# Performance work log

Measured on AMD Instinct MI355X. Metric: run time of the kernel, lower is better.

## Reference

```python
import jax, jax.numpy as jnp
import numpy as np
import math

SIZE = 64
NLAND = 8
N_ITER = 6


def setup_inputs() -> dict:
    key = jax.random.key(0)
    k1, k2, k3 = jax.random.split(key, 3)
    B, T, C = 4, 4096, 1024
    return {
        "q": jax.random.normal(k1, (B, T, C), dtype=jnp.float32),
        "k": jax.random.normal(k2, (B, T, C), dtype=jnp.float32),
        "v": jax.random.normal(k3, (B, T, C), dtype=jnp.float32),
    }


def _iterative_pinv(mat, n_iter=N_ITER):
    # Newton-Schulz iteration for pseudo-inverse of [..., m, m] kernel.
    m = mat.shape[-1]
    I = jnp.eye(m, dtype=mat.dtype)
    K = mat
    # NOTE: torch.max over the whole tensor (global scalar), faithful to source.
    V = (1.0 / jnp.max(jnp.sum(K, axis=-2))) * jnp.swapaxes(K, -1, -2)
    for _ in range(n_iter):
        KV = jnp.matmul(K, V)
        V = jnp.matmul(0.25 * V, 13.0 * I - jnp.matmul(KV, 15.0 * I - jnp.matmul(KV, 7.0 * I - KV)))
    return V


def reference(q, k, v):
    B, T, C = q.shape
    H = C // SIZE
    scale = 1.0 / math.sqrt(SIZE)
    # Faithful reshape (not transpose) as in the source module.
    qh = q.reshape(B, H, T, SIZE)
    kh = k.reshape(B, H, T, SIZE)
    vh = v.reshape(B, H, T, SIZE)
    # T % NLAND == 0 branch: landmark = segment mean over T//NLAND tokens.
    q_l = qh.reshape(B, H, NLAND, T // NLAND, SIZE).mean(axis=-2)  # [B,H,m,d]
    k_l = kh.reshape(B, H, NLAND, T // NLAND, SIZE).mean(axis=-2)
    kernel_1 = jax.nn.softmax(jnp.einsum('bhtd,bhmd->bhtm', qh, k_l) * scale, axis=-1)  # [B,H,T,m]
    kernel_2 = jax.nn.softmax(jnp.einsum('bhmd,bhnd->bhmn', q_l, k_l) * scale, axis=-1)  # [B,H,m,m]
    kernel_3 = jax.nn.softmax(jnp.einsum('bhmd,bhtd->bhmt', q_l, kh) * scale, axis=-1)  # [B,H,m,T]
    pinv = _iterative_pinv(kernel_2)  # [B,H,m,m]
    k3v = jnp.matmul(kernel_3, vh)    # [B,H,m,d]
    out = jnp.matmul(jnp.matmul(kernel_1, pinv), k3v)  # [B,H,T,d]
    return out.reshape(B, T, C)
```

## Files before the change

### kernel.cpp

```cpp
#include <hip/hip_runtime.h>
#include <math.h>

#define T_TOK 4096
#define DD 64
#define NHEADS 64
#define SEG 512
#define NCHUNK 32
#define CHUNK 128
#define SCALE 0.125f

#define QL_OFF   0
#define KL_OFF   32768
#define K2_OFF   65536
#define CS_OFF   69632
#define KP_OFF   70144
#define PA_OFF   70144
#define PD_OFF   1118720
#define W2_OFF   1135104
#define P_OFF    1167872

#define WAVE_BAR() __builtin_amdgcn_wave_barrier()

__global__ __launch_bounds__(256) void qsum_kernel(
    const float* __restrict__ q, float* __restrict__ ws) {
  int tid = threadIdx.x;
  const float4* q4 = (const float4*)q + (size_t)blockIdx.x * 8192;
  float4 b[2][8];
#pragma unroll
  for (int i = 0; i < 8; ++i) b[0][i] = q4[i * 256 + tid];
  float4 a = make_float4(0.f, 0.f, 0.f, 0.f);
#pragma unroll
  for (int j = 0; j < 4; ++j) {
    if (j < 3) {
#pragma unroll
      for (int i = 0; i < 8; ++i)
        b[(j + 1) & 1][i] = q4[(j + 1) * 2048 + i * 256 + tid];
    }
#pragma unroll
    for (int i = 0; i < 8; ++i) {
      float4 x = b[j & 1][i];
      a.x += x.x; a.y += x.y; a.z += x.z; a.w += x.w;
    }
  }
  __shared__ float4 red[16][17];
  red[tid >> 4][tid & 15] = a;
  __syncthreads();
  if (tid < 16) {
    float4 s = make_float4(0.f, 0.f, 0.f, 0.f);
#pragma unroll
    for (int g = 0; g < 16; ++g) {
      float4 r = red[g][tid];
      s.x += r.x; s.y += r.y; s.z += r.z; s.w += r.w;
    }
    const float inv = 1.f / (float)SEG;
    s.x *= inv; s.y *= inv; s.z *= inv; s.w *= inv;
    ((float4*)(ws + QL_OFF))[blockIdx.x * 16 + tid] = s;
  }
}

__global__ __launch_bounds__(256) void ppass_kernel(
    const float* __restrict__ k, float* __restrict__ ws) {
  int tid = threadIdx.x;
  int w = tid >> 6, lane = tid & 63;
  int gw = blockIdx.x * 4 + w;
  int hb = gw >> 6;
  __shared__ float kt_all[4][16][68];
  float (*kt)[68] = kt_all[w];

  int m = lane & 7;
  float4 qlrow[16];
#pragma unroll
  for (int d4 = 0; d4 < 16; ++d4)
    qlrow[d4] = ((const float4*)(ws + QL_OFF))[hb * 128 + m * 16 + d4];

  size_t tokbase = (size_t)gw * 64;
  const float4* k4 = (const float4*)k + tokbase * 16;
  float4 buf[2][4];
#pragma unroll
  for (int i = 0; i < 4; ++i) buf[0][i] = k4[i * 64 + lane];
  float4 ks = make_float4(0.f, 0.f, 0.f, 0.f);

#pragma unroll
  for (int tile = 0; tile < 4; ++tile) {
    int cur = tile & 1;
    if (tile < 3) {
#pragma unroll
      for (int i = 0; i < 4; ++i)
        buf[cur ^ 1][i] = k4[(tile + 1) * 256 + i * 64 + lane];
    }
#pragma unroll
    for (int i = 0; i < 4; ++i) {
      int f4 = i * 64 + lane;
      *(float4*)&kt[f4 >> 4][(f4 & 15) * 4] = buf[cur][i];
      ks.x += buf[cur][i].x; ks.y += buf[cur][i].y;
      ks.z += buf[cur][i].z; ks.w += buf[cur][i].w;
    }
    WAVE_BAR();
#pragma unroll
    for (int rep = 0; rep < 2; ++rep) {
      int t = rep * 8 + (lane >> 3);
      const float4* kr = (const float4*)&kt[t][0];
      float dp = 0.f;
#pragma unroll
      for (int d4 = 0; d4 < 16; ++d4) {
        float4 kv = kr[d4];
        dp += kv.x * qlrow[d4].x + kv.y * qlrow[d4].y +
              kv.z * qlrow[d4].z + kv.w * qlrow[d4].w;
      }
      ws[P_OFF + (tokbase + tile * 16 + t) * 8 + m] = __expf(dp * SCALE);
    }
    WAVE_BAR();
  }
  ks.x += __shfl_xor(ks.x, 16, 64); ks.y += __shfl_xor(ks.y, 16, 64);
  ks.z += __shfl_xor(ks.z, 16, 64); ks.w += __shfl_xor(ks.w, 16, 64);
  ks.x += __shfl_xor(ks.x, 32, 64); ks.y += __shfl_xor(ks.y, 32, 64);
  ks.z += __shfl_xor(ks.z, 32, 64); ks.w += __shfl_xor(ks.w, 32, 64);
  if (lane < 16)
    ((float4*)(ws + KP_OFF))[gw * 16 + lane] = ks;
}

__global__ __launch_bounds__(512) void prepk_kernel(float* __restrict__ ws) {
  int hb = blockIdx.x, tid = threadIdx.x;
  __shared__ float qls[8][68];
  __shared__ float kls[8][68];
  __shared__ float ee[8][9];
  int m = tid >> 6, d = tid & 63;
  float s = 0.f;
#pragma unroll
  for (int j = 0; j < 8; ++j)
    s += ws[KP_OFF + (size_t)(hb * 64 + m * 8 + j) * 64 + d];
  s *= (1.f / (float)SEG);
  kls[m][d] = s;
  ws[KL_OFF + hb * 512 + tid] = s;
  qls[m][d] = ws[QL_OFF + hb * 512 + tid];
  __syncthreads();
  if (tid < 64) {
    int i = tid >> 3, j = tid & 7;
    float dot = 0.f;
#pragma unroll
    for (int dd = 0; dd < 64; ++dd) dot += qls[i][dd] * kls[j][dd];
    ee[i][j] = __expf(dot * SCALE);
  }
  __syncthreads();
  if (tid < 64) {
    int i = tid >> 3, j = tid & 7;
    float ssum = 0.f;
#pragma unroll
    for (int jj = 0; jj < 8; ++jj) ssum += ee[i][jj];
    ws[K2_OFF + hb * 64 + tid] = ee[i][j] / ssum;
  }
  if (tid < 8) {
    float cs = 0.f;
    for (int ii = 0; ii < 8; ++ii) {
      float ssum = 0.f;
#pragma unroll
      for (int jj = 0; jj < 8; ++jj) ssum += ee[ii][jj];
      cs += ee[ii][tid] / ssum;
    }
    ws[CS_OFF + hb * 8 + tid] = cs;
  }
}

__global__ __launch_bounds__(256) void vpass_kernel(
    const float* __restrict__ v, float* __restrict__ ws) {
  int tid = threadIdx.x;
  int w = tid >> 6, lane = tid & 63, g = lane >> 4;
  int hb = blockIdx.x >> 5, c = blockIdx.x & 31;

  size_t tokbase = (size_t)hb * T_TOK + (size_t)c * CHUNK + (size_t)w * 32;
  float4 pf = ((const float4*)(ws + P_OFF))[tokbase * 2 + lane];
  const float4* v4 = (const float4*)v + tokbase * 16;
  float4 vv[8];
#pragma unroll
  for (int it = 0; it < 8; ++it) vv[it] = v4[it * 64 + lane];

  __shared__ float plds[4][260];
  *(float4*)&plds[w][lane * 4] = pf;
  WAVE_BAR();

  float4 acc[8];
#pragma unroll
  for (int m = 0; m < 8; ++m) acc[m] = make_float4(0.f, 0.f, 0.f, 0.f);

#pragma unroll
  for (int it = 0; it < 8; ++it) {
    int t = it * 4 + g;
    float4 pa = *(const float4*)&plds[w][t * 8];
    float4 pb = *(const float4*)&plds[w][t * 8 + 4];
    acc[0].x += pa.x * vv[it].x; acc[0].y += pa.x * vv[it].y; acc[0].z += pa.x * vv[it].z; acc[0].w += pa.x * vv[it].w;
    acc[1].x += pa.y * vv[it].x; acc[1].y += pa.y * vv[it].y; acc[1].z += pa.y * vv[it].z; acc[1].w += pa.y * vv[it].w;
    acc[2].x += pa.z * vv[it].x; acc[2].y += pa.z * vv[it].y; acc[2].z += pa.z * vv[it].z; acc[2].w += pa.z * vv[it].w;
    acc[3].x += pa.w * vv[it].x; acc[3].y += pa.w * vv[it].y; acc[3].z += pa.w * vv[it].z; acc[3].w += pa.w * vv[it].w;
    acc[4].x += pb.x * vv[it].x; acc[4].y += pb.x * vv[it].y; acc[4].z += pb.x * vv[it].z; acc[4].w += pb.x * vv[it].w;
    acc[5].x += pb.y * vv[it].x; acc[5].y += pb.y * vv[it].y; acc[5].z += pb.y * vv[it].z; acc[5].w += pb.y * vv[it].w;
    acc[6].x += pb.z * vv[it].x; acc[6].y += pb.z * vv[it].y; acc[6].z += pb.z * vv[it].z; acc[6].w += pb.z * vv[it].w;
    acc[7].x += pb.w * vv[it].x; acc[7].y += pb.w * vv[it].y; acc[7].z += pb.w * vv[it].z; acc[7].w += pb.w * vv[it].w;
  }
#pragma unroll
  for (int m = 0; m < 8; ++m) {
#pragma unroll
    for (int s = 16; s <= 32; s <<= 1) {
      acc[m].x += __shfl_xor(acc[m].x, s, 64);
      acc[m].y += __shfl_xor(acc[m].y, s, 64);
      acc[m].z += __shfl_xor(acc[m].z, s, 64);
      acc[m].w += __shfl_xor(acc[m].w, s, 64);
    }
  }
  __shared__ float4 accs[4][8][17];
  __shared__ float dens[4][8];
  if (lane < 16) {
#pragma unroll
    for (int m = 0; m < 8; ++m) accs[w][m][lane] = acc[m];
  }
  if (lane < 8) {
    float dsum = 0.f;
#pragma unroll
    for (int t = 0; t < 32; ++t) dsum += plds[w][t * 8 + lane];
    dens[w][lane] = dsum;
  }
  __syncthreads();
  if (tid < 128) {
    int m = tid >> 4, i = tid & 15;
    float4 a = accs[0][m][i], b = accs[1][m][i], cc = accs[2][m][i], dd = accs[3][m][i];
    float4 s = make_float4(a.x + b.x + cc.x + dd.x, a.y + b.y + cc.y + dd.y,
                           a.z + b.z + cc.z + dd.z, a.w + b.w + cc.w + dd.w);
    ((float4*)(ws + PA_OFF))[((size_t)(hb * 32 + c) * 8 + m) * 16 + i] = s;
  }
  if (tid < 8)
    ws[PD_OFF + (hb * NCHUNK + c) * 8 + tid] =
        dens[0][tid] + dens[1][tid] + dens[2][tid] + dens[3][tid];
}

__global__ __launch_bounds__(512) void pinvw2_kernel(float* __restrict__ ws) {
  int hb = blockIdx.x, tid = threadIdx.x;
  __shared__ float k3vs[8][68];
  __shared__ float K[8][9], V[8][9], X[8][9], Y[8][9];
  __shared__ float smax;
  int m = tid >> 6, d = tid & 63;
  float s = 0.f, den = 0.f;
  for (int c = 0; c < NCHUNK; ++c) {
    s += ws[PA_OFF + (((size_t)hb * NCHUNK + c) * 8 + m) * 64 + d];
    den += ws[PD_OFF + (hb * NCHUNK + c) * 8 + m];
  }
  k3vs[m][d] = s / den;
  if (tid < 64) {
    float mx = 0.f;
    for (int t = 0; t < 8; ++t) mx = fmaxf(mx, ws[CS_OFF + t * 64 + tid]);
    for (int off = 32; off; off >>= 1) mx = fmaxf(mx, __shfl_xor(mx, off, 64));
    if (tid == 0) smax = mx;
  }
  int i = (tid >> 3) & 7, j = tid & 7;
  if (tid < 64) K[i][j] = ws[K2_OFF + hb * 64 + tid];
  __syncthreads();
  if (tid < 64) V[i][j] = K[j][i] * (1.f / smax);
  __syncthreads();
  for (int it = 0; it < 6; ++it) {
    float x = 0.f;
    if (tid < 64) {
      for (int kk = 0; kk < 8; ++kk) x += K[i][kk] * V[kk][j];
      X[i][j] = x;
    }
    __syncthreads();
    float bm = 0.f;
    if (tid < 64) {
      for (int kk = 0; kk < 8; ++kk) bm += X[i][kk] * X[kk][j];
      bm = 7.f * x - bm;
      Y[i][j] = bm;
    }
    __syncthreads();
    float dm = 0.f;
    if (tid < 64) {
      for (int kk = 0; kk < 8; ++kk) dm += X[i][kk] * Y[kk][j];
      dm = 15.f * x - dm;
    }
    __syncthreads();
    if (tid < 64) Y[i][j] = dm;
    __syncthreads();
    float vd = 0.f;
    if (tid < 64) {
      for (int kk = 0; kk < 8; ++kk) vd += V[i][kk] * Y[kk][j];
      vd = 0.25f * (13.f * V[i][j] - vd);
    }
    __syncthreads();
    if (tid < 64) V[i][j] = vd;
    __syncthreads();
  }
  float o = 0.f;
#pragma unroll
  for (int jj = 0; jj < 8; ++jj) o += V[m][jj] * k3vs[jj][d];
  ws[W2_OFF + hb * 512 + tid] = o;
}

__global__ __launch_bounds__(256) void out_kernel(
    const float* __restrict__ q, float* __restrict__ out,
    const float* __restrict__ ws) {
  int tid = threadIdx.x;
  int w = tid >> 6, lane = tid & 63;
  int gw = blockIdx.x * 4 + w;
  int hb = gw >> 6;
  __shared__ float qt_all[4][16][68];
  __shared__ float pl_all[4][16][9];
  __shared__ float w2_all[4][8][68];
  float (*qt)[68] = qt_all[w];
  float (*pl)[9]  = pl_all[w];
  float (*w2)[68] = w2_all[w];

  int m = lane & 7;
  float4 klrow[16];
#pragma unroll
  for (int d4 = 0; d4 < 16; ++d4)
    klrow[d4] = ((const float4*)(ws + KL_OFF))[hb * 128 + m * 16 + d4];
#pragma unroll
  for (int i = 0; i < 2; ++i) {
    int f4 = i * 64 + lane;
    float4 y = ((const float4*)(ws + W2_OFF))[hb * 128 + f4];
    *(float4*)&w2[f4 >> 4][(f4 & 15) * 4] = y;
  }

  size_t base4 = (size_t)gw * 1024;
  const float4* q4 = (const float4*)q + base4;
  float4* o4 = (float4*)out + base4;
  float4 buf[2][4];
#pragma unroll
  for (int i = 0; i < 4; ++i) buf[0][i] = q4[i * 64 + lane];

#pragma unroll
  for (int tile = 0; tile < 4; ++tile) {
    int cur = tile & 1;
    if (tile < 3) {
#pragma unroll
      for (int i = 0; i < 4; ++i)
        buf[cur ^ 1][i] = q4[(tile + 1) * 256 + i * 64 + lane];
    }
#pragma unroll
    for (int i = 0; i < 4; ++i) {
      int f4 = i * 64 + lane;
      *(float4*)&qt[f4 >> 4][(f4 & 15) * 4] = buf[cur][i];
    }
    WAVE_BAR();
#pragma unroll
    for (int rep = 0; rep < 2; ++rep) {
      int t = rep * 8 + (lane >> 3);
      const float4* qr = (const float4*)&qt[t][0];
      float dot = 0.f;
#pragma unroll
      for (int d4 = 0; d4 < 16; ++d4) {
        float4 a = qr[d4];
        dot += a.x * klrow[d4].x + a.y * klrow[d4].y +
               a.z * klrow[d4].z + a.w * klrow[d4].w;
      }
      pl[t][m] = __expf(dot * SCALE);
    }
    WAVE_BAR();
#pragma unroll
    for (int i = 0; i < 4; ++i) {
      int t = i * 4 + (lane >> 4);
      int qd = lane & 15;
      float p0 = pl[t][0], p1 = pl[t][1], p2 = pl[t][2], p3 = pl[t][3];
      float p4 = pl[t][4], p5 = pl[t][5], p6 = pl[t][6], p7 = pl[t][7];
      float inv = 1.f / (p0 + p1 + p2 + p3 + p4 + p5 + p6 + p7);
      float4 acc = make_float4(0.f, 0.f, 0.f, 0.f);
      float pm[8] = {p0, p1, p2, p3, p4, p5, p6, p7};
#pragma unroll
      for (int m2 = 0; m2 < 8; ++m2) {
        float wgt = pm[m2] * inv;
        float4 wv = *(const float4*)&w2[m2][qd * 4];
        acc.x += wgt * wv.x; acc.y += wgt * wv.y;
        acc.z += wgt * wv.z; acc.w += wgt * wv.w;
      }
      o4[tile * 256 + i * 64 + lane] = acc;
    }
    WAVE_BAR();
  }
}

extern "C" void kernel_launch(void* const* d_in, const int* in_sizes, int n_in,
                              void* d_out, int out_size, void* d_ws, size_t ws_size,
                              hipStream_t stream) {
  const float* q = (const float*)d_in[0];
  const float* k = (const float*)d_in[1];
  const float* v = (const float*)d_in[2];
  float* out = (float*)d_out;
  float* ws = (float*)d_ws;

  qsum_kernel<<<512, 256, 0, stream>>>(q, ws);
  ppass_kernel<<<1024, 256, 0, stream>>>(k, ws);
  prepk_kernel<<<NHEADS, 512, 0, stream>>>(ws);
  vpass_kernel<<<NHEADS * NCHUNK, 256, 0, stream>>>(v, ws);
  pinvw2_kernel<<<NHEADS, 512, 0, stream>>>(ws);
  out_kernel<<<1024, 256, 0, stream>>>(q, out, ws);
}
```

Before: 88.76 us.

## Fuse K-score pass and V accumulation into a single kv-pass kernel

Merges the ppass and vpass kernels so each wave computes the exp scores for its 64 tokens and immediately accumulates the exp-weighted V sums and denominators, instead of writing the P matrix to workspace and reading it back in a separate launch. The landmark query rows now live in shared memory rather than registers, which frees registers for the new V buffers and accumulators. The intent is to remove one launch and the global round trip for P. The cost is more per-wave partials (64 per head instead of 32) for pinvw2 to reduce, and higher register pressure in the fused kernel.

```diff
diff --git a/kernel.cpp b/kernel.cpp
--- a/kernel.cpp
+++ b/kernel.cpp
@@ -5,8 +5,6 @@
 #define DD 64
 #define NHEADS 64
 #define SEG 512
-#define NCHUNK 32
-#define CHUNK 128
 #define SCALE 0.125f
 
 #define QL_OFF   0
@@ -14,10 +12,9 @@
 #define K2_OFF   65536
 #define CS_OFF   69632
 #define KP_OFF   70144
-#define PA_OFF   70144
-#define PD_OFF   1118720
-#define W2_OFF   1135104
-#define P_OFF    1167872
+#define PA_OFF   332288
+#define PD_OFF   2429440
+#define W2_OFF   2462208
 
 #define WAVE_BAR() __builtin_amdgcn_wave_barrier()
 
@@ -58,56 +55,87 @@
   }
 }
 
-__global__ __launch_bounds__(256) void ppass_kernel(
-    const float* __restrict__ k, float* __restrict__ ws) {
+__global__ __launch_bounds__(256) void kvpass_kernel(
+    const float* __restrict__ k, const float* __restrict__ v,
+    float* __restrict__ ws) {
   int tid = threadIdx.x;
   int w = tid >> 6, lane = tid & 63;
   int gw = blockIdx.x * 4 + w;
   int hb = gw >> 6;
+  __shared__ float qls[8][68];
   __shared__ float kt_all[4][16][68];
+  __shared__ float pl_all[4][16][9];
   float (*kt)[68] = kt_all[w];
-
-  int m = lane & 7;
-  float4 qlrow[16];
-#pragma unroll
-  for (int d4 = 0; d4 < 16; ++d4)
-    qlrow[d4] = ((const float4*)(ws + QL_OFF))[hb * 128 + m * 16 + d4];
-
+  float (*pl)[9]  = pl_all[w];
+
+  if (tid < 128) {
+    float4 x = ((const float4*)(ws + QL_OFF))[hb * 128 + tid];
+    *(float4*)&qls[tid >> 4][(tid & 15) * 4] = x;
+  }
+  __syncthreads();
+
+  int m = lane & 7, g = lane >> 4;
   size_t tokbase = (size_t)gw * 64;
   const float4* k4 = (const float4*)k + tokbase * 16;
-  float4 buf[2][4];
-#pragma unroll
-  for (int i = 0; i < 4; ++i) buf[0][i] = k4[i * 64 + lane];
+  const float4* v4 = (const float4*)v + tokbase * 16;
+  float4 kb[2][4], vb[2][4];
+#pragma unroll
+  for (int i = 0; i < 4; ++i) { kb[0][i] = k4[i * 64 + lane]; vb[0][i] = v4[i * 64 + lane]; }
+
   float4 ks = make_float4(0.f, 0.f, 0.f, 0.f);
+  float den = 0.f;
+  float4 acc[8];
+#pragma unroll
+  for (int mm = 0; mm < 8; ++mm) acc[mm] = make_float4(0.f, 0.f, 0.f, 0.f);
 
 #pragma unroll
   for (int tile = 0; tile < 4; ++tile) {
     int cur = tile & 1;
     if (tile < 3) {
 #pragma unroll
-      for (int i = 0; i < 4; ++i)
-        buf[cur ^ 1][i] = k4[(tile + 1) * 256 + i * 64 + lane];
+      for (int i = 0; i < 4; ++i) {
+        kb[cur ^ 1][i] = k4[(tile + 1) * 256 + i * 64 + lane];
+        vb[cur ^ 1][i] = v4[(tile + 1) * 256 + i * 64 + lane];
+      }
     }
 #pragma unroll
     for (int i = 0; i < 4; ++i) {
       int f4 = i * 64 + lane;
-      *(float4*)&kt[f4 >> 4][(f4 & 15) * 4] = buf[cur][i];
-      ks.x += buf[cur][i].x; ks.y += buf[cur][i].y;
-      ks.z += buf[cur][i].z; ks.w += buf[cur][i].w;
+      *(float4*)&kt[f4 >> 4][(f4 & 15) * 4] = kb[cur][i];
+      ks.x += kb[cur][i].x; ks.y += kb[cur][i].y;
+      ks.z += kb[cur][i].z; ks.w += kb[cur][i].w;
     }
     WAVE_BAR();
 #pragma unroll
     for (int rep = 0; rep < 2; ++rep) {
       int t = rep * 8 + (lane >> 3);
       const float4* kr = (const float4*)&kt[t][0];
+      const float4* qr = (const float4*)&qls[m][0];
       float dp = 0.f;
 #pragma unroll
       for (int d4 = 0; d4 < 16; ++d4) {
-        float4 kv = kr[d4];
-        dp += kv.x * qlrow[d4].x + kv.y * qlrow[d4].y +
-              kv.z * qlrow[d4].z + kv.w * qlrow[d4].w;
+        float4 kv = kr[d4], qv = qr[d4];
+        dp += kv.x * qv.x + kv.y * qv.y + kv.z * qv.z + kv.w * qv.w;
       }
-      ws[P_OFF + (tokbase + tile * 16 + t) * 8 + m] = __expf(dp * SCALE);
+      float p = __expf(dp * SCALE);
+      pl[t][m] = p;
+      den += p;
+    }
+    WAVE_BAR();
+#pragma unroll
+    for (int i = 0; i < 4; ++i) {
+      int t = i * 4 + g;
+      float4 vv = vb[cur][i];
+      float p0 = pl[t][0], p1 = pl[t][1], p2 = pl[t][2], p3 = pl[t][3];
+      float p4 = pl[t][4], p5 = pl[t][5], p6 = pl[t][6], p7 = pl[t][7];
+      acc[0].x += p0 * vv.x; acc[0].y += p0 * vv.y; acc[0].z += p0 * vv.z; acc[0].w += p0 * vv.w;
+      acc[1].x += p1 * vv.x; acc[1].y += p1 * vv.y; acc[1].z += p1 * vv.z; acc[1].w += p1 * vv.w;
+      acc[2].x += p2 * vv.x; acc[2].y += p2 * vv.y; acc[2].z += p2 * vv.z; acc[2].w += p2 * vv.w;
+      acc[3].x += p3 * vv.x; acc[3].y += p3 * vv.y; acc[3].z += p3 * vv.z; acc[3].w += p3 * vv.w;
+      acc[4].x += p4 * vv.x; acc[4].y += p4 * vv.y; acc[4].z += p4 * vv.z; acc[4].w += p4 * vv.w;
+      acc[5].x += p5 * vv.x; acc[5].y += p5 * vv.y; acc[5].z += p5 * vv.z; acc[5].w += p5 * vv.w;
+      acc[6].x += p6 * vv.x; acc[6].y += p6 * vv.y; acc[6].z += p6 * vv.z; acc[6].w += p6 * vv.w;
+      acc[7].x += p7 * vv.x; acc[7].y += p7 * vv.y; acc[7].z += p7 * vv.z; acc[7].w += p7 * vv.w;
     }
     WAVE_BAR();
   }
@@ -117,6 +145,26 @@
   ks.z += __shfl_xor(ks.z, 32, 64); ks.w += __shfl_xor(ks.w, 32, 64);
   if (lane < 16)
     ((float4*)(ws + KP_OFF))[gw * 16 + lane] = ks;
+  den += __shfl_xor(den, 8, 64);
+  den += __shfl_xor(den, 16, 64);
+  den += __shfl_xor(den, 32, 64);
+  if (lane < 8)
+    ws[PD_OFF + (size_t)gw * 8 + lane] = den;
+#pragma unroll
+  for (int mm = 0; mm < 8; ++mm) {
+#pragma unroll
+    for (int s = 16; s <= 32; s <<= 1) {
+      acc[mm].x += __shfl_xor(acc[mm].x, s, 64);
+      acc[mm].y += __shfl_xor(acc[mm].y, s, 64);
+      acc[mm].z += __shfl_xor(acc[mm].z, s, 64);
+      acc[mm].w += __shfl_xor(acc[mm].w, s, 64);
+    }
+  }
+  if (lane < 16) {
+#pragma unroll
+    for (int mm = 0; mm < 8; ++mm)
+      ((float4*)(ws + PA_OFF))[((size_t)gw * 8 + mm) * 16 + lane] = acc[mm];
+  }
 }
 
 __global__ __launch_bounds__(512) void prepk_kernel(float* __restrict__ ws) {
@@ -161,76 +209,6 @@
   }
 }
 
-__global__ __launch_bounds__(256) void vpass_kernel(
-    const float* __restrict__ v, float* __restrict__ ws) {
-  int tid = threadIdx.x;
-  int w = tid >> 6, lane = tid & 63, g = lane >> 4;
-  int hb = blockIdx.x >> 5, c = blockIdx.x & 31;
-
-  size_t tokbase = (size_t)hb * T_TOK + (size_t)c * CHUNK + (size_t)w * 32;
-  float4 pf = ((const float4*)(ws + P_OFF))[tokbase * 2 + lane];
-  const float4* v4 = (const float4*)v + tokbase * 16;
-  float4 vv[8];
-#pragma unroll
-  for (int it = 0; it < 8; ++it) vv[it] = v4[it * 64 + lane];
-
-  __shared__ float plds[4][260];
-  *(float4*)&plds[w][lane * 4] = pf;
-  WAVE_BAR();
-
-  float4 acc[8];
-#pragma unroll
-  for (int m = 0; m < 8; ++m) acc[m] = make_float4(0.f, 0.f, 0.f, 0.f);
-
-#pragma unroll
-  for (int it = 0; it < 8; ++it) {
-    int t = it * 4 + g;
-    float4 pa = *(const float4*)&plds[w][t * 8];
-    float4 pb = *(const float4*)&plds[w][t * 8 + 4];
-    acc[0].x += pa.x * vv[it].x; acc[0].y += pa.x * vv[it].y; acc[0].z += pa.x * vv[it].z; acc[0].w += pa.x * vv[it].w;
-    acc[1].x += pa.y * vv[it].x; acc[1].y += pa.y * vv[it].y; acc[1].z += pa.y * vv[it].z; acc[1].w += pa.y * vv[it].w;
-    acc[2].x += pa.z * vv[it].x; acc[2].y += pa.z * vv[it].y; acc[2].z += pa.z * vv[it].z; acc[2].w += pa.z * vv[it].w;
-    acc[3].x += pa.w * vv[it].x; acc[3].y += pa.w * vv[it].y; acc[3].z += pa.w * vv[it].z; acc[3].w += pa.w * vv[it].w;
-    acc[4].x += pb.x * vv[it].x; acc[4].y += pb.x * vv[it].y; acc[4].z += pb.x * vv[it].z; acc[4].w += pb.x * vv[it].w;
-    acc[5].x += pb.y * vv[it].x; acc[5].y += pb.y * vv[it].y; acc[5].z += pb.y * vv[it].z; acc[5].w += pb.y * vv[it].w;
-    acc[6].x += pb.z * vv[it].x; acc[6].y += pb.z * vv[it].y; acc[6].z += pb.z * vv[it].z; acc[6].w += pb.z * vv[it].w;
-    acc[7].x += pb.w * vv[it].x; acc[7].y += pb.w * vv[it].y; acc[7].z += pb.w * vv[it].z; acc[7].w += pb.w * vv[it].w;
-  }
-#pragma unroll
-  for (int m = 0; m < 8; ++m) {
-#pragma unroll
-    for (int s = 16; s <= 32; s <<= 1) {
-      acc[m].x += __shfl_xor(acc[m].x, s, 64);
-      acc[m].y += __shfl_xor(acc[m].y, s, 64);
-      acc[m].z += __shfl_xor(acc[m].z, s, 64);
-      acc[m].w += __shfl_xor(acc[m].w, s, 64);
-    }
-  }
-  __shared__ float4 accs[4][8][17];
-  __shared__ float dens[4][8];
-  if (lane < 16) {
-#pragma unroll
-    for (int m = 0; m < 8; ++m) accs[w][m][lane] = acc[m];
-  }
-  if (lane < 8) {
-    float dsum = 0.f;
-#pragma unroll
-    for (int t = 0; t < 32; ++t) dsum += plds[w][t * 8 + lane];
-    dens[w][lane] = dsum;
-  }
-  __syncthreads();
-  if (tid < 128) {
-    int m = tid >> 4, i = tid & 15;
-    float4 a = accs[0][m][i], b = accs[1][m][i], cc = accs[2][m][i], dd = accs[3][m][i];
-    float4 s = make_float4(a.x + b.x + cc.x + dd.x, a.y + b.y + cc.y + dd.y,
-                           a.z + b.z + cc.z + dd.z, a.w + b.w + cc.w + dd.w);
-    ((float4*)(ws + PA_OFF))[((size_t)(hb * 32 + c) * 8 + m) * 16 + i] = s;
-  }
-  if (tid < 8)
-    ws[PD_OFF + (hb * NCHUNK + c) * 8 + tid] =
-        dens[0][tid] + dens[1][tid] + dens[2][tid] + dens[3][tid];
-}
-
 __global__ __launch_bounds__(512) void pinvw2_kernel(float* __restrict__ ws) {
   int hb = blockIdx.x, tid = threadIdx.x;
   __shared__ float k3vs[8][68];
@@ -238,9 +216,9 @@
   __shared__ float smax;
   int m = tid >> 6, d = tid & 63;
   float s = 0.f, den = 0.f;
-  for (int c = 0; c < NCHUNK; ++c) {
-    s += ws[PA_OFF + (((size_t)hb * NCHUNK + c) * 8 + m) * 64 + d];
-    den += ws[PD_OFF + (hb * NCHUNK + c) * 8 + m];
+  for (int c = 0; c < 64; ++c) {
+    s += ws[PA_OFF + (((size_t)hb * 64 + c) * 8 + m) * 64 + d];
+    den += ws[PD_OFF + ((size_t)hb * 64 + c) * 8 + m];
   }
   k3vs[m][d] = s / den;
   if (tid < 64) {
@@ -384,9 +362,8 @@
   float* ws = (float*)d_ws;
 
   qsum_kernel<<<512, 256, 0, stream>>>(q, ws);
-  ppass_kernel<<<1024, 256, 0, stream>>>(k, ws);
+  kvpass_kernel<<<1024, 256, 0, stream>>>(k, v, ws);
   prepk_kernel<<<NHEADS, 512, 0, stream>>>(ws);
-  vpass_kernel<<<NHEADS * NCHUNK, 256, 0, stream>>>(v, ws);
   pinvw2_kernel<<<NHEADS, 512, 0, stream>>>(ws);
   out_kernel<<<1024, 256, 0, stream>>>(q, out, ws);
 }
```

New measurement: 99.14 us. 11.7% more time.
